# Kernel optimization log

Hardware: AMD Instinct MI355X
Metric: run time of the kernel (lower is better)

Reference implementation:

```python
import jax, jax.numpy as jnp
import numpy as np

E = 500_000
N_ENT = 100_000
N_REL = 237
IN_DIM = 100
OUT_DIM = 100
BN_EPS = 1e-5


def _batchnorm(x, gamma, beta):
    # torch BatchNorm1d training-mode normalization (biased variance)
    mu = jnp.mean(x, axis=0)
    var = jnp.var(x, axis=0)
    return (x - mu) * jax.lax.rsqrt(var + BN_EPS) * gamma + beta


def setup_inputs() -> dict:
    key = jax.random.key(0)
    ks = jax.random.split(key, 8)
    heads = jax.random.randint(ks[0], (E,), 0, N_ENT)
    tails = jax.random.randint(ks[1], (E,), 0, N_ENT)
    rels = jax.random.randint(ks[2], (E,), 0, N_REL)
    triplets = jnp.stack([heads, tails, rels], axis=1)  # [E,3] int
    ent_embed = jax.random.normal(ks[3], (N_ENT, IN_DIM), jnp.float32) * 0.1
    rel_embed = jax.random.normal(ks[4], (N_REL, IN_DIM), jnp.float32) * 0.1
    a_W = jax.random.normal(ks[5], (OUT_DIM, 3 * IN_DIM), jnp.float32) * (1.414 / np.sqrt(3 * IN_DIM))
    a_b = jnp.zeros((OUT_DIM,), jnp.float32)
    a2_W = jax.random.normal(ks[6], (1, OUT_DIM), jnp.float32) * (1.414 / np.sqrt(OUT_DIM))
    a2_b = jnp.zeros((1,), jnp.float32)
    return {
        "triplets": triplets,
        "ent_embed": ent_embed,
        "rel_embed": rel_embed,
        "a_W": a_W,
        "a_b": a_b,
        "a2_W": a2_W,
        "a2_b": a2_b,
        "bn0_g": jnp.ones((3 * IN_DIM,), jnp.float32),
        "bn0_b": jnp.zeros((3 * IN_DIM,), jnp.float32),
        "bn1_g": jnp.ones((OUT_DIM,), jnp.float32),
        "bn1_b": jnp.zeros((OUT_DIM,), jnp.float32),
    }


def reference(triplets, ent_embed, rel_embed, a_W, a_b, a2_W, a2_b,
              bn0_g, bn0_b, bn1_g, bn1_b):
    t0, t1, t2 = triplets[:, 0], triplets[:, 1], triplets[:, 2]
    E_ = triplets.shape[0]
    N = ent_embed.shape[0]
    R = rel_embed.shape[0]

    # gather + concat: forward and inverse triples -> [2E, 3*in_dim]
    h_fwd = jnp.concatenate([ent_embed[t0], ent_embed[t1], rel_embed[t2]], axis=1)
    h_inv = jnp.concatenate([ent_embed[t1], ent_embed[t0], -rel_embed[t2]], axis=1)
    h = jnp.concatenate([h_fwd, h_inv], axis=0)

    h = _batchnorm(h, bn0_g, bn0_b)          # bn0 (dropout p used in eval/identity)
    c = _batchnorm(h @ a_W.T + a_b, bn1_g, bn1_b)  # [2E, out]
    b = -jax.nn.leaky_relu(c @ a2_W.T + a2_b, 0.01)  # [2E, 1]
    e_b = jnp.exp(b)                          # [2E, 1]

    # sparse neighborhood aggregation = segment-sum over edge source node
    src = jnp.concatenate([t0, t1])           # [2E]
    ebs = jax.ops.segment_sum(e_b, src, num_segments=N)          # [N,1]
    temp1 = e_b * c                                               # [2E,out]
    hs = jax.ops.segment_sum(temp1, src, num_segments=N)         # [N,out]
    ebs = jnp.where(ebs == 0, 1e-12, ebs)
    h_ent = hs / ebs

    # relation update: scatter-mean over relation index, fwd minus inverse
    cnt = jax.ops.segment_sum(jnp.ones((E_,), temp1.dtype), t2, num_segments=R)
    cnt = jnp.maximum(cnt, 1.0)[:, None]
    h_rel = (jax.ops.segment_sum(temp1[:E_], t2, num_segments=R)
             - jax.ops.segment_sum(temp1[E_:], t2, num_segments=R)) / cnt

    return jax.nn.elu(h_ent), jax.nn.elu(h_rel)
```

## Files before the change

### kernel.cpp

```cpp
#include <hip/hip_runtime.h>
#include <hip/hip_bf16.h>

#define E_EDGES 500000
#define NENT    100000
#define NREL    237
#define DIM     100
#define TDIM    300
#define TWO_E   1000000
#define BN_EPS  1e-5f
#define PITCH   256
#define NB      512
#define CHUNK   977
#define RSEG    16
#define ECHUNK  391

typedef unsigned short u16;
typedef unsigned int   u32;
typedef unsigned long long u64;

static const size_t OFF_DEG     = 0;
static const size_t OFF_CUR     = 100000;
static const size_t OFF_S1      = 200000;
static const size_t OFF_S2      = 200128;
static const size_t OFF_S2R     = 200256;
static const size_t OFF_SC      = 200384;
static const size_t OFF_SC2     = 200512;
static const size_t OFF_CONST   = 200640;
static const size_t OFF_RELACC  = 200704;
static const size_t ZERO_END    = 224448;
static const size_t OFF_OFFS    = 224448;
static const size_t OFF_ROFF    = 324464;
static const size_t OFF_RELCNTF = 324704;
static const size_t OFF_BHIST   = 324960;
static const size_t OFF_RBASE   = 456032;
static const size_t OFF_PART    = 577376;
static const size_t OFF_BASE    = 577632;
static const size_t OFF_RTOT    = 577888;
static const size_t OFF_SCALE0  = 578144;
static const size_t OFF_SHIFT0  = 578464;
static const size_t OFF_BP      = 578784;
static const size_t OFF_SCALE1  = 578912;
static const size_t OFF_SHIFT1  = 579040;
static const size_t OFF_WVEC    = 579168;
static const size_t OFF_WPT     = 579296;
static const size_t OFF_WRELT   = 599296;
static const size_t OFF_V       = 609296;
static const size_t OFF_PSI     = 633040;
static const size_t OFF_PHI0    = 633296;
static const size_t OFF_PHI1    = 733296;
static const size_t OFF_RELE64  = 833296;
static const size_t OFF_INC     = 1833296;
static const size_t OFF_UE      = 2833296;
static const size_t TOTAL_F     = 15633296;

__device__ __forceinline__ float bf2f(u16 u){ return __uint_as_float(((u32)u)<<16); }
__device__ __forceinline__ u16 f2bf(float f){
  u32 x = __float_as_uint(f);
  x += 0x7FFFu + ((x>>16)&1u);
  return (u16)(x>>16);
}
__device__ __forceinline__ void ld4a(const u16* p, float* o){
  ushort4 u = *(const ushort4*)p;
  o[0]=bf2f(u.x); o[1]=bf2f(u.y); o[2]=bf2f(u.z); o[3]=bf2f(u.w);
}
__device__ __forceinline__ void ld4f(const float* p, float* o){
  float4 v = *(const float4*)p;
  o[0]=v.x; o[1]=v.y; o[2]=v.z; o[3]=v.w;
}
__device__ __forceinline__ float eluf(float v){ return v>0.f ? v : expf(v)-1.f; }
__device__ __forceinline__ float ewt(float t){ return expf( t>0.f ? -t : -0.01f*t ); }

__global__ __launch_bounds__(256) void k_histA(const int* __restrict__ trip,
                                               u32* __restrict__ deg, u32* __restrict__ bhist){
  __shared__ u32 lh[256];
  int t = threadIdx.x, b = blockIdx.x;
  lh[t] = 0u;
  __syncthreads();
  int e0 = b*CHUNK, e1 = e0+CHUNK; if (e1 > E_EDGES) e1 = E_EDGES;
  for (int e=e0+t; e<e1; e+=256){
    int3 tr = ((const int3*)trip)[e];
    atomicAdd(&deg[tr.x], 1u);
    atomicAdd(&deg[tr.y], 1u);
    atomicAdd(&lh[tr.z], 1u);
  }
  __syncthreads();
  bhist[b*256 + t] = lh[t];
}

__global__ __launch_bounds__(256) void k_scanA(const u32* __restrict__ deg, u32* __restrict__ part){
  __shared__ u32 red[256];
  int b = blockIdx.x, t = threadIdx.x;
  int c0 = b*ECHUNK, c1 = c0+ECHUNK; if (c1 > NENT) c1 = NENT; if (c0 > NENT) c0 = NENT;
  u32 s=0;
  for (int n=c0+t; n<c1; n+=256) s += deg[n];
  red[t]=s; __syncthreads();
  for (int m=128;m>=1;m>>=1){ if (t<m) red[t]+=red[t+m]; __syncthreads(); }
  if (t==0) part[b]=red[0];
}

__global__ __launch_bounds__(256) void k_scanR(const u32* __restrict__ bhist,
                                               u32* __restrict__ rbase, u32* __restrict__ rtot){
  __shared__ u32 sd[256];
  int r = blockIdx.x, t = threadIdx.x;
  u32 v0 = bhist[(size_t)(2*t)*256 + r];
  u32 v1 = bhist[(size_t)(2*t+1)*256 + r];
  u32 v = v0+v1;
  sd[t]=v; __syncthreads();
  for (int o=1;o<256;o<<=1){ u32 x=(t>=o)?sd[t-o]:0u; __syncthreads(); sd[t]+=x; __syncthreads(); }
  u32 ex = sd[t]-v;
  rbase[(size_t)r*NB + 2*t]   = ex;
  rbase[(size_t)r*NB + 2*t+1] = ex+v0;
  if (t==255) rtot[r] = sd[255];
}

__global__ __launch_bounds__(256) void k_scanB(const u32* __restrict__ part, u32* __restrict__ base,
                                               u32* __restrict__ offs,
                                               const u32* __restrict__ rtot, u32* __restrict__ roff,
                                               float* __restrict__ relcntf){
  __shared__ u32 sd[256];
  int t = threadIdx.x;
  u32 v = part[t];
  sd[t]=v; __syncthreads();
  for (int o=1;o<256;o<<=1){ u32 x=(t>=o)?sd[t-o]:0u; __syncthreads(); sd[t]+=x; __syncthreads(); }
  base[t] = sd[t]-v;
  if (t==255) offs[NENT] = sd[255];
  __syncthreads();
  u32 rv = (t<NREL)? rtot[t] : 0u;
  sd[t]=rv; __syncthreads();
  for (int o=1;o<256;o<<=1){ u32 x=(t>=o)?sd[t-o]:0u; __syncthreads(); sd[t]+=x; __syncthreads(); }
  if (t<NREL){ roff[t]=sd[t]-rv; relcntf[t]=(float)rv; }
  if (t==NREL-1) roff[NREL]=sd[t];
}

__global__ __launch_bounds__(256) void k_scanC(const u32* __restrict__ deg, const u32* __restrict__ base,
                                               u32* __restrict__ offs){
  __shared__ u32 sd[256];
  int b = blockIdx.x, t = threadIdx.x;
  int c0 = b*ECHUNK;
  int cend = c0+ECHUNK; if (cend > NENT) cend = NENT;
  int n0 = c0 + 2*t;
  u32 d0 = (n0   < cend)? deg[n0]   : 0u;
  u32 d1 = (n0+1 < cend)? deg[n0+1] : 0u;
  u32 v = d0+d1;
  sd[t]=v; __syncthreads();
  for (int o=1;o<256;o<<=1){ u32 x=(t>=o)?sd[t-o]:0u; __syncthreads(); sd[t]+=x; __syncthreads(); }
  u32 ex = base[b] + sd[t]-v;
  if (n0   < cend) offs[n0]   = ex;
  if (n0+1 < cend) offs[n0+1] = ex+d0;
}

__global__ __launch_bounds__(256) void k_incB(const int* __restrict__ trip,
                      const u32* __restrict__ offs, u32* __restrict__ cur,
                      const u32* __restrict__ roff, const u32* __restrict__ rbase,
                      u32* __restrict__ inc, u64* __restrict__ rele64){
  __shared__ u32 lh[256];
  int t = threadIdx.x, b = blockIdx.x;
  lh[t] = 0u;
  __syncthreads();
  int e0 = b*CHUNK, e1 = e0+CHUNK; if (e1 > E_EDGES) e1 = E_EDGES;
  for (int e=e0+t; e<e1; e+=256){
    int3 tr = ((const int3*)trip)[e];
    u32 p0 = offs[tr.x] + atomicAdd(&cur[tr.x], 1u);
    inc[p0] = (u32)tr.y | ((u32)tr.z<<17);
    u32 p1 = offs[tr.y] + atomicAdd(&cur[tr.y], 1u);
    inc[p1] = (u32)tr.x | ((u32)tr.z<<17) | (1u<<25);
    u32 loff = atomicAdd(&lh[tr.z], 1u);
    rele64[roff[tr.z] + rbase[(u32)tr.z*NB + b] + loff] = (u64)(u32)tr.x | ((u64)(u32)tr.y<<17);
  }
}

__global__ void k_entstats(const float* __restrict__ ent, const u32* __restrict__ deg,
                           float* __restrict__ S1, float* __restrict__ S2){
  int d = threadIdx.x;
  if (d >= DIM) return;
  int n0 = blockIdx.x*256;
  int nend = n0+256; if (nend > NENT) nend = NENT;
  float s1=0.f, s2=0.f;
  for (int n=n0;n<nend;n++){
    float w = (float)deg[n];
    float x = ent[(size_t)n*DIM + d];
    s1 += w*x; s2 += w*x*x;
  }
  atomicAdd(&S1[d], s1);
  atomicAdd(&S2[d], s2);
}

__global__ void k_relstats(const float* __restrict__ rel, const float* __restrict__ relcnt, float* __restrict__ S2r){
  int d = threadIdx.x;
  if (d >= DIM) return;
  float s=0.f;
  for (int r=0;r<NREL;r++){
    float x = rel[r*DIM+d];
    s += relcnt[r]*x*x;
  }
  S2r[d] = s;
}

__global__ void k_scale0(const float* __restrict__ g0, const float* __restrict__ b0,
                         const float* __restrict__ S1, const float* __restrict__ S2, const float* __restrict__ S2r,
                         float* __restrict__ scale0, float* __restrict__ shift0){
  int j = threadIdx.x;
  if (j >= TDIM) return;
  float mean, var;
  if (j < 200){
    int d = (j<100)? j : j-100;
    mean = S1[d] * (1.0f/TWO_E);
    var  = S2[d] * (1.0f/TWO_E) - mean*mean;
  } else {
    mean = 0.0f;
    var  = S2r[j-200] * (1.0f/E_EDGES);
  }
  float sc = g0[j] * rsqrtf(var + BN_EPS);
  scale0[j] = sc;
  shift0[j] = b0[j] - mean*sc;
}

__global__ void k_foldW(const float* __restrict__ aW, const float* __restrict__ scale0,
                        float* __restrict__ Wpt, float* __restrict__ Wrelt){
  int idx = blockIdx.x*256 + threadIdx.x;
  if (idx < 20000){
    int d = idx/200, kk = idx%200;
    int k = (kk<100)? kk : kk-100;
    int j = (kk<100)? d : 100+d;
    Wpt[idx] = aW[k*TDIM + j] * scale0[j];
  } else if (idx < 30000){
    int i2 = idx - 20000;
    int d = i2/100, k = i2%100;
    Wrelt[i2] = aW[k*TDIM + 200 + d] * scale0[200+d];
  }
}

__global__ void k_bp(const float* __restrict__ aW, const float* __restrict__ ab,
                     const float* __restrict__ shift0, float* __restrict__ bp){
  int k = blockIdx.x;
  int l = threadIdx.x;
  float s=0.f;
  for (int j=l;j<TDIM;j+=64) s += aW[k*TDIM+j] * shift0[j];
  #pragma unroll
  for (int m=32;m>=1;m>>=1) s += __shfl_xor(s, m, 64);
  if (l==0) bp[k] = s + ab[k];
}

__global__ void k_V(const float* __restrict__ rel, const float* __restrict__ Wrelt, float* __restrict__ V){
  __shared__ float rf[DIM];
  int r = blockIdx.x;
  int k = threadIdx.x;
  if (k < DIM) rf[k] = rel[r*DIM+k];
  __syncthreads();
  if (k >= DIM) return;
  float s=0.f;
  for (int d=0;d<DIM;d++) s += Wrelt[d*DIM+k]*rf[d];
  V[r*DIM+k] = s;
}

__global__ __launch_bounds__(256) void k_U(const float* __restrict__ ent, const float* __restrict__ Wpt,
                                           u16* __restrict__ UEp){
  __shared__ float sh[DIM][36];
  int n0 = blockIdx.x*32;
  for (int idx=threadIdx.x; idx<32*DIM; idx+=256){
    int n = idx/DIM, d = idx%DIM;
    sh[d][n] = ent[(size_t)(n0+n)*DIM + d];
  }
  __syncthreads();
  int kk = threadIdx.x;
  if (kk >= 200) return;
  float acc[32];
  #pragma unroll
  for (int i=0;i<32;i++) acc[i]=0.f;
  for (int d=0;d<DIM;d++){
    float w = Wpt[d*200+kk];
    #pragma unroll
    for (int i=0;i<32;i++) acc[i] += w*sh[d][i];
  }
  int col = (kk<100)? kk : (28+kk);
  for (int i=0;i<32;i++) UEp[(size_t)(n0+i)*PITCH + col] = f2bf(acc[i]);
}

__global__ __launch_bounds__(256) void k_cstats(const int* __restrict__ trip,
    const u16* __restrict__ UEp, const float* __restrict__ V, const float* __restrict__ bp,
    float* __restrict__ Sc, float* __restrict__ Sc2){
  __shared__ float scB[DIM], sc2B[DIM];
  for (int i=threadIdx.x;i<DIM;i+=256){ scB[i]=0.f; sc2B[i]=0.f; }
  __syncthreads();
  int lane = threadIdx.x & 31;
  int slot = (blockIdx.x*256 + threadIdx.x) >> 5;
  int nslots = gridDim.x*8;
  bool act = lane < 25;
  int dbase = lane*4;
  float bpv[4]={0,0,0,0};
  if (act) ld4f(bp+dbase, bpv);
  float sc[4]={0,0,0,0}, sc2[4]={0,0,0,0};
  for (int e=slot; e<E_EDGES; e+=nslots){
    int3 t = ((const int3*)trip)[e];
    if (act){
      const u16* rx = UEp + (size_t)t.x*PITCH;
      const u16* ry = UEp + (size_t)t.y*PITCH;
      float P[4],Q[4],R[4],S[4],Vv[4];
      ld4a(rx+dbase, P);
      ld4a(ry+128+dbase, Q);
      ld4a(ry+dbase, R);
      ld4a(rx+128+dbase, S);
      ld4f(V+(size_t)t.z*DIM+dbase, Vv);
      #pragma unroll
      for (int i=0;i<4;i++){
        float cf = P[i]+Q[i]+Vv[i]+bpv[i];
        float ci = R[i]+S[i]-Vv[i]+bpv[i];
        sc[i]  += cf+ci;
        sc2[i] += cf*cf + ci*ci;
      }
    }
  }
  if (act){
    #pragma unroll
    for (int i=0;i<4;i++){ atomicAdd(&scB[dbase+i], sc[i]); atomicAdd(&sc2B[dbase+i], sc2[i]); }
  }
  __syncthreads();
  for (int i=threadIdx.x;i<DIM;i+=256){ atomicAdd(&Sc[i], scB[i]); atomicAdd(&Sc2[i], sc2B[i]); }
}

__global__ void k_bn1x(const float* __restrict__ g1, const float* __restrict__ b1,
                       const float* __restrict__ Sc, const float* __restrict__ Sc2,
                       const float* __restrict__ bp, const float* __restrict__ a2W, const float* __restrict__ a2b,
                       float* __restrict__ scale1, float* __restrict__ shift1,
                       float* __restrict__ wvec, float* __restrict__ consts){
  __shared__ float red[128];
  int k = threadIdx.x;
  float contrib = 0.f;
  if (k < DIM){
    float mean = Sc[k]*(1.0f/TWO_E);
    float var  = Sc2[k]*(1.0f/TWO_E) - mean*mean;
    float s = g1[k] * rsqrtf(var + BN_EPS);
    float sh = b1[k] - mean*s;
    float a2 = a2W[k];
    scale1[k] = s;
    shift1[k] = sh;
    float wv = s*a2;
    wvec[k] = wv;
    contrib = bp[k]*wv + sh*a2;
  }
  red[k] = contrib;
  __syncthreads();
  for (int m=64;m>=1;m>>=1){ if (k<m) red[k]+=red[k+m]; __syncthreads(); }
  if (k==0) consts[0] = red[0] + a2b[0];
}

__global__ __launch_bounds__(256) void k_phi(const u16* __restrict__ UEp, const float* __restrict__ wvec,
                                             float* __restrict__ phi0, float* __restrict__ phi1){
  int lane = threadIdx.x & 31;
  int n = blockIdx.x*8 + (threadIdx.x>>5);
  bool act = lane < 25;
  int dbase = lane*4;
  float w4[4]={0,0,0,0};
  float p0=0.f, p1=0.f;
  if (act){
    ld4f(wvec+dbase, w4);
    float P[4], Q[4];
    ld4a(UEp + (size_t)n*PITCH + dbase, P);
    ld4a(UEp + (size_t)n*PITCH + 128 + dbase, Q);
    #pragma unroll
    for (int i=0;i<4;i++){ p0 += P[i]*w4[i]; p1 += Q[i]*w4[i]; }
  }
  #pragma unroll
  for (int m=16;m>=1;m>>=1){ p0 += __shfl_xor(p0,m,32); p1 += __shfl_xor(p1,m,32); }
  if (lane==0){ phi0[n]=p0; phi1[n]=p1; }
}

__global__ void k_psi(const float* __restrict__ V, const float* __restrict__ wvec, float* __restrict__ psi){
  __shared__ float w[DIM];
  int t = threadIdx.x;
  if (t < DIM) w[t] = wvec[t];
  __syncthreads();
  if (t >= NREL) return;
  float s=0.f;
  for (int k=0;k<DIM;k++) s += V[t*DIM+k]*w[k];
  psi[t] = s;
}

__global__ __launch_bounds__(256) void k_aggr_ent(const u32* __restrict__ offs, const u32* __restrict__ inc,
    const u16* __restrict__ UEp, const float* __restrict__ V,
    const float* __restrict__ phi0, const float* __restrict__ phi1, const float* __restrict__ psi,
    const float* __restrict__ consts, const float* __restrict__ bp,
    const float* __restrict__ scale1, const float* __restrict__ shift1,
    float* __restrict__ out){
  int lane = threadIdx.x & 31;
  int n = blockIdx.x*8 + (threadIdx.x>>5);
  bool act = lane < 25;
  int dbase = lane*4;
  u32 o0 = offs[n], o1 = offs[n+1];
  float C = consts[0];
  float p0n = phi0[n];
  float acc[4]={0,0,0,0};
  float wsum=0.f;
  for (u32 i=o0; i<o1; i++){
    u32 pk = inc[i];
    u32 other = pk & 0x1FFFFu;
    u32 rr = (pk>>17) & 0xFFu;
    bool neg = (pk>>25) != 0u;
    float ps = psi[rr];
    float t = p0n + phi1[other] + (neg ? -ps : ps) + C;
    float w = ewt(t);
    wsum += w;
    if (act){
      float B[4], Vv[4];
      ld4a(UEp + (size_t)other*PITCH + 128 + dbase, B);
      ld4f(V + (size_t)rr*DIM + dbase, Vv);
      float sg = neg ? -1.f : 1.f;
      #pragma unroll
      for (int i2=0;i2<4;i2++) acc[i2] += w*(B[i2]+sg*Vv[i2]);
    }
  }
  if (act){
    float o4[4];
    if (o1 == o0){
      o4[0]=o4[1]=o4[2]=o4[3]=0.f;
    } else {
      float P[4], bp4[4], s14[4], sh4[4];
      ld4a(UEp + (size_t)n*PITCH + dbase, P);
      ld4f(bp+dbase, bp4);
      ld4f(scale1+dbase, s14);
      ld4f(shift1+dbase, sh4);
      float inv = __frcp_rn(wsum);
      #pragma unroll
      for (int i2=0;i2<4;i2++){
        float v = (P[i2]+bp4[i2])*s14[i2] + sh4[i2] + s14[i2]*acc[i2]*inv;
        o4[i2] = eluf(v);
      }
    }
    *(float4*)(out + (size_t)n*DIM + dbase) = make_float4(o4[0],o4[1],o4[2],o4[3]);
  }
}

__global__ __launch_bounds__(256) void k_aggr_relP(
    const u32* __restrict__ roff, const u64* __restrict__ rele64,
    const u16* __restrict__ UEp, const float* __restrict__ V,
    const float* __restrict__ phi0, const float* __restrict__ phi1, const float* __restrict__ psi,
    const float* __restrict__ consts, const float* __restrict__ bp,
    const float* __restrict__ scale1, const float* __restrict__ shift1,
    float* __restrict__ relacc){
  __shared__ float red[8][104];
  int r   = blockIdx.x / RSEG;
  int seg = blockIdx.x % RSEG;
  int lane = threadIdx.x & 31;
  int slot = threadIdx.x >> 5;
  bool act = lane < 25;
  int dbase = lane*4;
  float C = consts[0];
  float psir = psi[r];
  float bp4[4]={0,0,0,0}, s14[4]={0,0,0,0}, sh4[4]={0,0,0,0}, Vv[4]={0,0,0,0};
  if (act){
    ld4f(bp+dbase, bp4);
    ld4f(scale1+dbase, s14);
    ld4f(shift1+dbase, sh4);
    ld4f(V + (size_t)r*DIM + dbase, Vv);
  }
  u32 q0 = roff[r], q1 = roff[r+1];
  float acc[4]={0,0,0,0};
  for (u32 q = q0 + (u32)(seg*8+slot); q < q1; q += RSEG*8){
    u64 pk = rele64[q];
    u32 t0 = (u32)(pk & 0x1FFFFu);
    u32 t1 = (u32)((pk>>17) & 0x1FFFFu);
    float tf = phi0[t0] + phi1[t1] + psir + C;
    float ti = phi0[t1] + phi1[t0] - psir + C;
    float ef = ewt(tf);
    float ei = ewt(ti);
    if (act){
      const u16* rx = UEp + (size_t)t0*PITCH;
      const u16* ry = UEp + (size_t)t1*PITCH;
      float P[4],Q[4],R[4],S[4];
      ld4a(rx+dbase, P);
      ld4a(ry+128+dbase, Q);
      ld4a(ry+dbase, R);
      ld4a(rx+128+dbase, S);
      #pragma unroll
      for (int i=0;i<4;i++){
        float cf = (P[i]+Q[i]+Vv[i]+bp4[i])*s14[i] + sh4[i];
        float ci = (R[i]+S[i]-Vv[i]+bp4[i])*s14[i] + sh4[i];
        acc[i] += ef*cf - ei*ci;
      }
    }
  }
  if (act){
    #pragma unroll
    for (int i=0;i<4;i++) red[slot][dbase+i] = acc[i];
  }
  __syncthreads();
  int k = threadIdx.x;
  if (k < DIM){
    float s = 0.f;
    #pragma unroll
    for (int sl=0;sl<8;sl++) s += red[sl][k];
    atomicAdd(&relacc[(size_t)r*DIM + k], s);
  }
}

__global__ void k_out_rel(const float* __restrict__ relacc, const float* __restrict__ relcnt,
                          float* __restrict__ out){
  int idx = blockIdx.x*256 + threadIdx.x;
  if (idx >= NREL*DIM) return;
  int r = idx/DIM;
  float cn = relcnt[r]; if (cn < 1.f) cn = 1.f;
  out[(size_t)NENT*DIM + idx] = eluf(relacc[idx]/cn);
}

extern "C" void kernel_launch(void* const* d_in, const int* in_sizes, int n_in,
                              void* d_out, int out_size, void* d_ws, size_t ws_size,
                              hipStream_t stream){
  const int*   trip = (const int*)d_in[0];
  const float* ent  = (const float*)d_in[1];
  const float* rel  = (const float*)d_in[2];
  const float* aW   = (const float*)d_in[3];
  const float* ab   = (const float*)d_in[4];
  const float* a2W  = (const float*)d_in[5];
  const float* a2b  = (const float*)d_in[6];
  const float* g0   = (const float*)d_in[7];
  const float* b0   = (const float*)d_in[8];
  const float* g1   = (const float*)d_in[9];
  const float* b1   = (const float*)d_in[10];
  float* out = (float*)d_out;
  float* wsf = (float*)d_ws;
  if (ws_size < TOTAL_F*sizeof(float)) return;
  u16* UEp  = (u16*)(wsf + OFF_UE);
  u32* deg  = (u32*)(wsf + OFF_DEG);
  u32* cur  = (u32*)(wsf + OFF_CUR);
  u32* offs = (u32*)(wsf + OFF_OFFS);
  u32* roff = (u32*)(wsf + OFF_ROFF);
  u32* bhist= (u32*)(wsf + OFF_BHIST);
  u32* rbase= (u32*)(wsf + OFF_RBASE);
  u32* part = (u32*)(wsf + OFF_PART);
  u32* base = (u32*)(wsf + OFF_BASE);
  u32* rtot = (u32*)(wsf + OFF_RTOT);
  u32* inc  = (u32*)(wsf + OFF_INC);
  u64* rele = (u64*)(wsf + OFF_RELE64);

  hipMemsetAsync(d_ws, 0, ZERO_END*sizeof(float), stream);

  k_histA<<<dim3(NB), dim3(256), 0, stream>>>(trip, deg, bhist);
  k_entstats<<<dim3((NENT+255)/256), dim3(128), 0, stream>>>(ent, deg, wsf+OFF_S1, wsf+OFF_S2);
  k_scanA<<<dim3(256), dim3(256), 0, stream>>>(deg, part);
  k_scanR<<<dim3(NREL), dim3(256), 0, stream>>>(bhist, rbase, rtot);
  k_scanB<<<dim3(1), dim3(256), 0, stream>>>(part, base, offs, rtot, roff, wsf+OFF_RELCNTF);
  k_scanC<<<dim3(256), dim3(256), 0, stream>>>(deg, base, offs);
  k_relstats<<<dim3(1), dim3(128), 0, stream>>>(rel, wsf+OFF_RELCNTF, wsf+OFF_S2R);
  k_scale0<<<dim3(1), dim3(320), 0, stream>>>(g0, b0, wsf+OFF_S1, wsf+OFF_S2, wsf+OFF_S2R,
                                              wsf+OFF_SCALE0, wsf+OFF_SHIFT0);
  k_foldW<<<dim3(118), dim3(256), 0, stream>>>(aW, wsf+OFF_SCALE0, wsf+OFF_WPT, wsf+OFF_WRELT);
  k_bp<<<dim3(100), dim3(64), 0, stream>>>(aW, ab, wsf+OFF_SHIFT0, wsf+OFF_BP);
  k_V<<<dim3(NREL), dim3(128), 0, stream>>>(rel, wsf+OFF_WRELT, wsf+OFF_V);
  k_U<<<dim3(NENT/32), dim3(256), 0, stream>>>(ent, wsf+OFF_WPT, UEp);
  k_incB<<<dim3(NB), dim3(256), 0, stream>>>(trip, offs, cur, roff, rbase, inc, rele);
  k_cstats<<<dim3(2048), dim3(256), 0, stream>>>(trip, UEp, wsf+OFF_V, wsf+OFF_BP,
                                                 wsf+OFF_SC, wsf+OFF_SC2);
  k_bn1x<<<dim3(1), dim3(128), 0, stream>>>(g1, b1, wsf+OFF_SC, wsf+OFF_SC2, wsf+OFF_BP, a2W, a2b,
                                            wsf+OFF_SCALE1, wsf+OFF_SHIFT1, wsf+OFF_WVEC, wsf+OFF_CONST);
  k_phi<<<dim3(NENT/8), dim3(256), 0, stream>>>(UEp, wsf+OFF_WVEC, wsf+OFF_PHI0, wsf+OFF_PHI1);
  k_psi<<<dim3(1), dim3(256), 0, stream>>>(wsf+OFF_V, wsf+OFF_WVEC, wsf+OFF_PSI);
  k_aggr_ent<<<dim3(NENT/8), dim3(256), 0, stream>>>(offs, inc, UEp, wsf+OFF_V,
                                                     wsf+OFF_PHI0, wsf+OFF_PHI1, wsf+OFF_PSI,
                                                     wsf+OFF_CONST, wsf+OFF_BP,
                                                     wsf+OFF_SCALE1, wsf+OFF_SHIFT1, out);
  k_aggr_relP<<<dim3(NREL*RSEG), dim3(256), 0, stream>>>(roff, rele, UEp, wsf+OFF_V,
                                                   wsf+OFF_PHI0, wsf+OFF_PHI1, wsf+OFF_PSI,
                                                   wsf+OFF_CONST, wsf+OFF_BP,
                                                   wsf+OFF_SCALE1, wsf+OFF_SHIFT1,
                                                   wsf+OFF_RELACC);
  k_out_rel<<<dim3((NREL*DIM+255)/256), dim3(256), 0, stream>>>(wsf+OFF_RELACC, wsf+OFF_RELCNTF, out);
}
```

Measured before the change: 668.1 us.

## Compute BN1 stats per source node via CSR and unroll aggregation loops by two

The BN1 statistics kernel now walks the per-entity incidence list instead of the raw triplet array. Each warp loads its own node's row halves once and skips inverse entries, which removes two of the four random row gathers per edge. The entity and relation aggregation loops are also unrolled by two so that more independent gathers are in flight at once. In exchange, the stats kernel inherits degree imbalance across warps, and the unrolled loops use more registers.

Result: slower. 834.4 us (+24.9%).

```diff
diff --git a/kernel.cpp b/kernel.cpp
--- a/kernel.cpp
+++ b/kernel.cpp
@@ -276,43 +276,49 @@
   for (int i=0;i<32;i++) UEp[(size_t)(n0+i)*PITCH + col] = f2bf(acc[i]);
 }
 
-__global__ __launch_bounds__(256) void k_cstats(const int* __restrict__ trip,
+__global__ __launch_bounds__(256) void k_cstats2(const u32* __restrict__ offs, const u32* __restrict__ inc,
     const u16* __restrict__ UEp, const float* __restrict__ V, const float* __restrict__ bp,
     float* __restrict__ Sc, float* __restrict__ Sc2){
   __shared__ float scB[DIM], sc2B[DIM];
   for (int i=threadIdx.x;i<DIM;i+=256){ scB[i]=0.f; sc2B[i]=0.f; }
   __syncthreads();
   int lane = threadIdx.x & 31;
-  int slot = (blockIdx.x*256 + threadIdx.x) >> 5;
-  int nslots = gridDim.x*8;
+  int n = blockIdx.x*8 + (threadIdx.x>>5);
   bool act = lane < 25;
   int dbase = lane*4;
-  float bpv[4]={0,0,0,0};
-  if (act) ld4f(bp+dbase, bpv);
+  u32 o0 = offs[n], o1 = offs[n+1];
+  float bpv[4]={0,0,0,0}, P4[4]={0,0,0,0}, S4[4]={0,0,0,0};
+  if (act){
+    ld4f(bp+dbase, bpv);
+    if (o1 > o0){
+      ld4a(UEp + (size_t)n*PITCH + dbase, P4);
+      ld4a(UEp + (size_t)n*PITCH + 128 + dbase, S4);
+    }
+  }
   float sc[4]={0,0,0,0}, sc2[4]={0,0,0,0};
-  for (int e=slot; e<E_EDGES; e+=nslots){
-    int3 t = ((const int3*)trip)[e];
+  for (u32 i=o0;i<o1;i++){
+    u32 pk = inc[i];
+    if (pk & (1u<<25)) continue;
+    u32 other = pk & 0x1FFFFu;
+    u32 rr = (pk>>17)&0xFFu;
     if (act){
-      const u16* rx = UEp + (size_t)t.x*PITCH;
-      const u16* ry = UEp + (size_t)t.y*PITCH;
-      float P[4],Q[4],R[4],S[4],Vv[4];
-      ld4a(rx+dbase, P);
+      const u16* ry = UEp + (size_t)other*PITCH;
+      float Q[4],R[4],Vv[4];
       ld4a(ry+128+dbase, Q);
       ld4a(ry+dbase, R);
-      ld4a(rx+128+dbase, S);
-      ld4f(V+(size_t)t.z*DIM+dbase, Vv);
+      ld4f(V+(size_t)rr*DIM+dbase, Vv);
       #pragma unroll
-      for (int i=0;i<4;i++){
-        float cf = P[i]+Q[i]+Vv[i]+bpv[i];
-        float ci = R[i]+S[i]-Vv[i]+bpv[i];
-        sc[i]  += cf+ci;
-        sc2[i] += cf*cf + ci*ci;
+      for (int j=0;j<4;j++){
+        float cf = P4[j]+Q[j]+Vv[j]+bpv[j];
+        float ci = R[j]+S4[j]-Vv[j]+bpv[j];
+        sc[j]  += cf+ci;
+        sc2[j] += cf*cf+ci*ci;
       }
     }
   }
   if (act){
     #pragma unroll
-    for (int i=0;i<4;i++){ atomicAdd(&scB[dbase+i], sc[i]); atomicAdd(&sc2B[dbase+i], sc2[i]); }
+    for (int j=0;j<4;j++){ atomicAdd(&scB[dbase+j], sc[j]); atomicAdd(&sc2B[dbase+j], sc2[j]); }
   }
   __syncthreads();
   for (int i=threadIdx.x;i<DIM;i+=256){ atomicAdd(&Sc[i], scB[i]); atomicAdd(&Sc2[i], sc2B[i]); }
@@ -391,22 +397,44 @@
   float p0n = phi0[n];
   float acc[4]={0,0,0,0};
   float wsum=0.f;
-  for (u32 i=o0; i<o1; i++){
+  u32 i = o0;
+  for (; i+2 <= o1; i += 2){
+    u32 pk0 = inc[i], pk1 = inc[i+1];
+    u32 oth0 = pk0 & 0x1FFFFu,      oth1 = pk1 & 0x1FFFFu;
+    u32 rr0  = (pk0>>17) & 0xFFu,   rr1  = (pk1>>17) & 0xFFu;
+    float sg0 = (pk0>>25)? -1.f:1.f, sg1 = (pk1>>25)? -1.f:1.f;
+    float ph0 = phi1[oth0], ph1 = phi1[oth1];
+    float ps0 = psi[rr0],   ps1 = psi[rr1];
+    float B0[4],V0[4],B1[4],V1[4];
+    if (act){
+      ld4a(UEp + (size_t)oth0*PITCH + 128 + dbase, B0);
+      ld4a(UEp + (size_t)oth1*PITCH + 128 + dbase, B1);
+      ld4f(V + (size_t)rr0*DIM + dbase, V0);
+      ld4f(V + (size_t)rr1*DIM + dbase, V1);
+    }
+    float t0 = p0n + ph0 + sg0*ps0 + C;
+    float t1 = p0n + ph1 + sg1*ps1 + C;
+    float w0 = ewt(t0), w1 = ewt(t1);
+    wsum += w0+w1;
+    if (act){
+      #pragma unroll
+      for (int j=0;j<4;j++) acc[j] += w0*(B0[j]+sg0*V0[j]) + w1*(B1[j]+sg1*V1[j]);
+    }
+  }
+  if (i < o1){
     u32 pk = inc[i];
-    u32 other = pk & 0x1FFFFu;
+    u32 oth = pk & 0x1FFFFu;
     u32 rr = (pk>>17) & 0xFFu;
-    bool neg = (pk>>25) != 0u;
-    float ps = psi[rr];
-    float t = p0n + phi1[other] + (neg ? -ps : ps) + C;
+    float sg = (pk>>25)? -1.f:1.f;
+    float t = p0n + phi1[oth] + sg*psi[rr] + C;
     float w = ewt(t);
     wsum += w;
     if (act){
       float B[4], Vv[4];
-      ld4a(UEp + (size_t)other*PITCH + 128 + dbase, B);
+      ld4a(UEp + (size_t)oth*PITCH + 128 + dbase, B);
       ld4f(V + (size_t)rr*DIM + dbase, Vv);
-      float sg = neg ? -1.f : 1.f;
       #pragma unroll
-      for (int i2=0;i2<4;i2++) acc[i2] += w*(B[i2]+sg*Vv[i2]);
+      for (int j=0;j<4;j++) acc[j] += w*(B[j]+sg*Vv[j]);
     }
   }
   if (act){
@@ -421,9 +449,9 @@
       ld4f(shift1+dbase, sh4);
       float inv = __frcp_rn(wsum);
       #pragma unroll
-      for (int i2=0;i2<4;i2++){
-        float v = (P[i2]+bp4[i2])*s14[i2] + sh4[i2] + s14[i2]*acc[i2]*inv;
-        o4[i2] = eluf(v);
+      for (int j=0;j<4;j++){
+        float v = (P[j]+bp4[j])*s14[j] + sh4[j] + s14[j]*acc[j]*inv;
+        o4[j] = eluf(v);
       }
     }
     *(float4*)(out + (size_t)n*DIM + dbase) = make_float4(o4[0],o4[1],o4[2],o4[3]);
@@ -455,33 +483,44 @@
   }
   u32 q0 = roff[r], q1 = roff[r+1];
   float acc[4]={0,0,0,0};
-  for (u32 q = q0 + (u32)(seg*8+slot); q < q1; q += RSEG*8){
-    u64 pk = rele64[q];
-    u32 t0 = (u32)(pk & 0x1FFFFu);
-    u32 t1 = (u32)((pk>>17) & 0x1FFFFu);
-    float tf = phi0[t0] + phi1[t1] + psir + C;
-    float ti = phi0[t1] + phi1[t0] - psir + C;
-    float ef = ewt(tf);
-    float ei = ewt(ti);
+  for (u32 q = q0 + (u32)(seg*8+slot)*2; q < q1; q += (u32)(RSEG*8*2)){
+    u64 pk0 = rele64[q];
+    bool has1 = (q+1 < q1);
+    u64 pk1 = has1 ? rele64[q+1] : pk0;
+    u32 a0 = (u32)(pk0 & 0x1FFFFu), b0 = (u32)((pk0>>17) & 0x1FFFFu);
+    u32 a1 = (u32)(pk1 & 0x1FFFFu), b1 = (u32)((pk1>>17) & 0x1FFFFu);
+    float P0[4],Q0[4],R0[4],S0[4],P1[4],Q1[4],R1[4],S1[4];
     if (act){
-      const u16* rx = UEp + (size_t)t0*PITCH;
-      const u16* ry = UEp + (size_t)t1*PITCH;
-      float P[4],Q[4],R[4],S[4];
-      ld4a(rx+dbase, P);
-      ld4a(ry+128+dbase, Q);
-      ld4a(ry+dbase, R);
-      ld4a(rx+128+dbase, S);
+      const u16* rx0 = UEp + (size_t)a0*PITCH;
+      const u16* ry0 = UEp + (size_t)b0*PITCH;
+      const u16* rx1 = UEp + (size_t)a1*PITCH;
+      const u16* ry1 = UEp + (size_t)b1*PITCH;
+      ld4a(rx0+dbase, P0);      ld4a(ry0+128+dbase, Q0);
+      ld4a(ry0+dbase, R0);      ld4a(rx0+128+dbase, S0);
+      ld4a(rx1+dbase, P1);      ld4a(ry1+128+dbase, Q1);
+      ld4a(ry1+dbase, R1);      ld4a(rx1+128+dbase, S1);
+    }
+    float tf0 = phi0[a0] + phi1[b0] + psir + C;
+    float ti0 = phi0[b0] + phi1[a0] - psir + C;
+    float tf1 = phi0[a1] + phi1[b1] + psir + C;
+    float ti1 = phi0[b1] + phi1[a1] - psir + C;
+    float m1 = has1 ? 1.f : 0.f;
+    float ef0 = ewt(tf0), ei0 = ewt(ti0);
+    float ef1 = m1*ewt(tf1), ei1 = m1*ewt(ti1);
+    if (act){
       #pragma unroll
-      for (int i=0;i<4;i++){
-        float cf = (P[i]+Q[i]+Vv[i]+bp4[i])*s14[i] + sh4[i];
-        float ci = (R[i]+S[i]-Vv[i]+bp4[i])*s14[i] + sh4[i];
-        acc[i] += ef*cf - ei*ci;
+      for (int j=0;j<4;j++){
+        float cf0 = (P0[j]+Q0[j]+Vv[j]+bp4[j])*s14[j] + sh4[j];
+        float ci0 = (R0[j]+S0[j]-Vv[j]+bp4[j])*s14[j] + sh4[j];
+        float cf1 = (P1[j]+Q1[j]+Vv[j]+bp4[j])*s14[j] + sh4[j];
+        float ci1 = (R1[j]+S1[j]-Vv[j]+bp4[j])*s14[j] + sh4[j];
+        acc[j] += ef0*cf0 - ei0*ci0 + ef1*cf1 - ei1*ci1;
       }
     }
   }
   if (act){
     #pragma unroll
-    for (int i=0;i<4;i++) red[slot][dbase+i] = acc[i];
+    for (int j=0;j<4;j++) red[slot][dbase+j] = acc[j];
   }
   __syncthreads();
   int k = threadIdx.x;
@@ -548,8 +587,8 @@
   k_V<<<dim3(NREL), dim3(128), 0, stream>>>(rel, wsf+OFF_WRELT, wsf+OFF_V);
   k_U<<<dim3(NENT/32), dim3(256), 0, stream>>>(ent, wsf+OFF_WPT, UEp);
   k_incB<<<dim3(NB), dim3(256), 0, stream>>>(trip, offs, cur, roff, rbase, inc, rele);
-  k_cstats<<<dim3(2048), dim3(256), 0, stream>>>(trip, UEp, wsf+OFF_V, wsf+OFF_BP,
-                                                 wsf+OFF_SC, wsf+OFF_SC2);
+  k_cstats2<<<dim3(NENT/8), dim3(256), 0, stream>>>(offs, inc, UEp, wsf+OFF_V, wsf+OFF_BP,
+                                                    wsf+OFF_SC, wsf+OFF_SC2);
   k_bn1x<<<dim3(1), dim3(128), 0, stream>>>(g1, b1, wsf+OFF_SC, wsf+OFF_SC2, wsf+OFF_BP, a2W, a2b,
                                             wsf+OFF_SCALE1, wsf+OFF_SHIFT1, wsf+OFF_WVEC, wsf+OFF_CONST);
   k_phi<<<dim3(NENT/8), dim3(256), 0, stream>>>(UEp, wsf+OFF_WVEC, wsf+OFF_PHI0, wsf+OFF_PHI1);
```
